# Kernel tuning notes

Measured on AMD Instinct MI355X. Metric: run time of the kernel, lower is better.

## Reference

```python
import jax, jax.numpy as jnp
import numpy as np

EPS = 1e-7  # tf.keras.backend.epsilon()


def squash(v, axis=-1):
    s = jnp.sum(jnp.square(v), axis=axis, keepdims=True)
    scale = s / (1.0 + s) / jnp.sqrt(s + EPS)
    return scale * v


def setup_inputs() -> dict:
    key = jax.random.key(0)
    k1, k2 = jax.random.split(key)
    B, I, D = 64, 2048, 16   # batch, input_num_capsule, input_dim_capsule
    J, K = 32, 16            # num_capsule, dim_capsule
    inputs = jax.random.normal(k1, (B, I, D), dtype=jnp.float32)
    # glorot_uniform-ish init for W: [in_caps, num_caps, in_dim, dim_caps]
    limit = np.sqrt(6.0 / (D + K)).astype(np.float32)
    W = jax.random.uniform(k2, (I, J, D, K), dtype=jnp.float32, minval=-limit, maxval=limit)
    return {"inputs": inputs, "W": W}


def reference(inputs, W, routings=3):
    # u_hat[b,i,j,:] = inputs[b,i,:] @ W[i,j,:,:]
    u_hat = jnp.einsum('bid,ijdk->bijk', inputs, W)  # [B, I, J, K]
    B, I, J, _ = u_hat.shape
    b = jnp.zeros((B, I, J, 1), dtype=u_hat.dtype)
    outputs = None
    for r in range(routings):
        c = jax.nn.softmax(b, axis=2)                              # [B, I, J, 1]
        outputs = squash(jnp.sum(c * u_hat, axis=1, keepdims=True))  # [B, 1, J, K]
        if r < routings - 1:
            b = b + jnp.sum(u_hat * outputs, axis=-1, keepdims=True)
    return jnp.squeeze(outputs, axis=1)  # [B, J, K]
```

## Files before the change

kernel.cpp:

```cpp
#include <hip/hip_runtime.h>
#include <hip/hip_bf16.h>


#define B_ 64
#define I_ 2048
#define D_ 16
#define J_ 32
#define K_ 16
#define JK 512

__device__ __forceinline__ float bf2f(unsigned int u) {
    union { unsigned int i; float f; } v;
    v.i = u << 16;
    return v.f;
}

__device__ __forceinline__ unsigned short f2bf(float f) {
    union { float f; unsigned int i; } v;
    v.f = f;
    const unsigned int x = v.i;
    return (unsigned short)((x + 0x7fffu + ((x >> 16) & 1u)) >> 16);
}

__device__ __forceinline__ void unpack8(const uint4 r, float* u) {
    u[0] = bf2f(r.x & 0xffffu); u[1] = bf2f(r.x >> 16);
    u[2] = bf2f(r.y & 0xffffu); u[3] = bf2f(r.y >> 16);
    u[4] = bf2f(r.z & 0xffffu); u[5] = bf2f(r.z >> 16);
    u[6] = bf2f(r.w & 0xffffu); u[7] = bf2f(r.w >> 16);
}

__global__ __launch_bounds__(64)
void caps_probe(const unsigned short* __restrict__ x, int* __restrict__ flag) {
    const int lane = threadIdx.x;
    int wild = 0;
#pragma unroll 8
    for (int t = 0; t < 128; ++t) {
        const unsigned int u = x[(size_t)lane * 128 + t];
        const unsigned int e = (u >> 7) & 0xffu;
        wild += (e >= 0xC0u) ? 1 : 0;
    }
    wild += __shfl_xor(wild, 1, 64);
    wild += __shfl_xor(wild, 2, 64);
    wild += __shfl_xor(wild, 4, 64);
    wild += __shfl_xor(wild, 8, 64);
    wild += __shfl_xor(wild, 16, 64);
    wild += __shfl_xor(wild, 32, 64);
    if (lane == 0) *flag = (wild > 32) ? 1 : 0;
}

__global__ __launch_bounds__(512)
void caps_produce(const void* __restrict__ xv, const void* __restrict__ Wv,
                  unsigned short* __restrict__ uhat, int b0, int BT,
                  const int* __restrict__ flag) {
    __shared__ float lx[4][64][D_];
    const int tid = threadIdx.x;
    const int g = tid >> 7;
    const int st = tid & 127;
    const int i = (blockIdx.x << 2) | g;
    const bool F32 = (*flag != 0);

    if (st < BT * 2) {
        const int bl = st >> 1, h = st & 1;
        float tmp[8];
        if (F32) {
            const float* xp =
                (const float*)xv + ((size_t)(b0 + bl) * I_ + i) * D_ + h * 8;
            const float4 r0 = reinterpret_cast<const float4*>(xp)[0];
            const float4 r1 = reinterpret_cast<const float4*>(xp)[1];
            tmp[0] = r0.x; tmp[1] = r0.y; tmp[2] = r0.z; tmp[3] = r0.w;
            tmp[4] = r1.x; tmp[5] = r1.y; tmp[6] = r1.z; tmp[7] = r1.w;
        } else {
            const uint4 r = *reinterpret_cast<const uint4*>(
                (const unsigned short*)xv +
                ((size_t)(b0 + bl) * I_ + i) * D_ + h * 8);
            unpack8(r, tmp);
        }
        float4* dst = reinterpret_cast<float4*>(&lx[g][bl][h * 8]);
        float4 d0, d1;
        d0.x = tmp[0]; d0.y = tmp[1]; d0.z = tmp[2]; d0.w = tmp[3];
        d1.x = tmp[4]; d1.y = tmp[5]; d1.z = tmp[6]; d1.w = tmp[7];
        dst[0] = d0; dst[1] = d1;
    }

    float w[16][4];
    {
        const int j = st >> 2, kh = st & 3;
        if (F32) {
            const float* wp = (const float*)Wv + (size_t)i * (J_ * D_ * K_) +
                              j * (D_ * K_) + kh * 4;
#pragma unroll
            for (int d = 0; d < 16; ++d) {
                const float4 r = *reinterpret_cast<const float4*>(wp + d * K_);
                w[d][0] = r.x; w[d][1] = r.y; w[d][2] = r.z; w[d][3] = r.w;
            }
        } else {
            const unsigned short* wp = (const unsigned short*)Wv +
                                       (size_t)i * (J_ * D_ * K_) +
                                       j * (D_ * K_) + kh * 4;
#pragma unroll
            for (int d = 0; d < 16; ++d) {
                const uint2 r = *reinterpret_cast<const uint2*>(wp + d * K_);
                w[d][0] = bf2f(r.x & 0xffffu); w[d][1] = bf2f(r.x >> 16);
                w[d][2] = bf2f(r.y & 0xffffu); w[d][3] = bf2f(r.y >> 16);
            }
        }
    }
    __syncthreads();

#pragma unroll 2
    for (int bl = 0; bl < BT; ++bl) {
        const float4* xr = reinterpret_cast<const float4*>(&lx[g][bl][0]);
        float a[4] = {0.f, 0.f, 0.f, 0.f};
#pragma unroll
        for (int dq = 0; dq < 4; ++dq) {
            const float4 xq = xr[dq];
            const float xs[4] = {xq.x, xq.y, xq.z, xq.w};
#pragma unroll
            for (int dd = 0; dd < 4; ++dd) {
#pragma unroll
                for (int c = 0; c < 4; ++c) a[c] += xs[dd] * w[dq * 4 + dd][c];
            }
        }
        uint2 pk;
        pk.x = ((unsigned int)f2bf(a[1]) << 16) | f2bf(a[0]);
        pk.y = ((unsigned int)f2bf(a[3]) << 16) | f2bf(a[2]);
        *reinterpret_cast<uint2*>(
            uhat + ((size_t)bl * I_ + i) * JK + st * 4) = pk;
    }
}

template <bool R0>
__global__ __launch_bounds__(256)
void caps_route(const unsigned short* __restrict__ uhat,
                const float* __restrict__ vsum,
                float* __restrict__ spart, int BT) {
    const int lane = threadIdx.x & 63;
    const int wave = blockIdx.x * 4 + (threadIdx.x >> 6);
    const int bl = wave >> 6;
    const int chunk = wave & 63;
    const int i0 = chunk * 32;

    float v[8];
    if (!R0) {
        const float4* vp =
            reinterpret_cast<const float4*>(vsum + bl * JK + lane * 8);
        const float4 v0 = vp[0], v1 = vp[1];
        v[0] = v0.x; v[1] = v0.y; v[2] = v0.z; v[3] = v0.w;
        v[4] = v1.x; v[5] = v1.y; v[6] = v1.z; v[7] = v1.w;
    }

    float acc[8] = {0.f, 0.f, 0.f, 0.f, 0.f, 0.f, 0.f, 0.f};
    const unsigned short* up = uhat + ((size_t)bl * I_ + i0) * JK + lane * 8;

#pragma unroll 2
    for (int ii = 0; ii < 32; ++ii) {
        const uint4 r = *reinterpret_cast<const uint4*>(up + (size_t)ii * JK);
        float u[8];
        unpack8(r, u);
        float c;
        if (R0) {
            c = 1.f;
        } else {
            float p = u[0] * v[0] + u[1] * v[1] + u[2] * v[2] + u[3] * v[3] +
                      u[4] * v[4] + u[5] * v[5] + u[6] * v[6] + u[7] * v[7];
            const float t = p + __shfl_xor(p, 1, 64);
            const float e = __expf(t);
            float S = e;
            S += __shfl_xor(S, 2, 64);
            S += __shfl_xor(S, 4, 64);
            S += __shfl_xor(S, 8, 64);
            S += __shfl_xor(S, 16, 64);
            S += __shfl_xor(S, 32, 64);
            c = e / S;
        }
#pragma unroll
        for (int q = 0; q < 8; ++q) acc[q] += c * u[q];
    }

    float* sp = spart + ((size_t)chunk * BT + bl) * JK + lane * 8;
    float4 o0, o1;
    o0.x = acc[0]; o0.y = acc[1]; o0.z = acc[2]; o0.w = acc[3];
    o1.x = acc[4]; o1.y = acc[5]; o1.z = acc[6]; o1.w = acc[7];
    reinterpret_cast<float4*>(sp)[0] = o0;
    reinterpret_cast<float4*>(sp)[1] = o1;
}

template <int MODE>
__global__ __launch_bounds__(512)
void caps_squash(const float* __restrict__ spart, float* __restrict__ vsum,
                 void* __restrict__ out, int b0, int BT,
                 const int* __restrict__ flag) {
    const int bl = blockIdx.x;
    const int jk = threadIdx.x;
    float s = 0.f;
#pragma unroll 8
    for (int p = 0; p < 64; ++p)
        s += spart[((size_t)p * BT + bl) * JK + jk];
    if (MODE == 0) s *= (1.f / 32.f);
    float q = s * s;
    q += __shfl_xor(q, 1, 64);
    q += __shfl_xor(q, 2, 64);
    q += __shfl_xor(q, 4, 64);
    q += __shfl_xor(q, 8, 64);
    const float scale = q / ((1.f + q) * sqrtf(q + 1e-7f));
    const float v = scale * s;
    if (MODE == 0)      vsum[bl * JK + jk] = v;
    else if (MODE == 1) vsum[bl * JK + jk] += v;
    else {
        const size_t o = (size_t)(b0 + bl) * JK + jk;
        if (*flag) ((float*)out)[o] = v;
        else       ((unsigned short*)out)[o] = f2bf(v);
    }
}

extern "C" void kernel_launch(void* const* d_in, const int* in_sizes, int n_in,
                              void* d_out, int out_size, void* d_ws,
                              size_t ws_size, hipStream_t stream) {
    const void* x = d_in[0];
    const void* W = d_in[1];
    char* ws = (char*)d_ws;

    int BT = 64;
    auto need = [](int bt) -> size_t {
        return (size_t)bt * I_ * JK * 2
             + (size_t)64 * bt * JK * 4
             + (size_t)bt * JK * 4
             + 256;
    };
    while (BT > 1 && need(BT) > ws_size) BT >>= 1;

    unsigned short* uhat = (unsigned short*)ws;
    float* spart = (float*)(ws + (size_t)BT * I_ * JK * 2);
    float* vsum = spart + (size_t)64 * BT * JK;
    int* flag = (int*)(vsum + (size_t)BT * JK);

    caps_probe<<<1, 64, 0, stream>>>((const unsigned short*)x, flag);

    const int NT = B_ / BT;
    for (int t = 0; t < NT; ++t) {
        const int b0 = t * BT;
        caps_produce<<<I_ / 4, 512, 0, stream>>>(x, W, uhat, b0, BT, flag);

        caps_route<true><<<BT * 16, 256, 0, stream>>>(uhat, vsum, spart, BT);
        caps_squash<0><<<BT, 512, 0, stream>>>(spart, vsum, d_out, b0, BT, flag);

        caps_route<false><<<BT * 16, 256, 0, stream>>>(uhat, vsum, spart, BT);
        caps_squash<1><<<BT, 512, 0, stream>>>(spart, vsum, d_out, b0, BT, flag);

        caps_route<false><<<BT * 16, 256, 0, stream>>>(uhat, vsum, spart, BT);
        caps_squash<2><<<BT, 512, 0, stream>>>(spart, vsum, d_out, b0, BT, flag);
    }
}
```

Before: 229.4 us.

## Drop LDS staging in produce and remap route lanes to whole capsules

The produce kernel no longer stages x through shared memory with a barrier. Each wave now loads the 16-element x row for its input capsule directly, using a readfirstlane-uniform index, and blocks shrink to 256 threads. The route kernel gives each lane a full 16-wide capsule j, with the two wave halves handling alternating i rows. This removes the pairwise shuffle for the dot product and folds the halves with one final shuffle. The trade-offs are more registers per lane, fewer concurrent i rows per block, and redundant x loads across lanes, which should be served as broadcasts.

New measurement: 245.7 us. 7.1% more time.

```diff
diff --git a/kernel.cpp b/kernel.cpp
--- a/kernel.cpp
+++ b/kernel.cpp
@@ -48,39 +48,16 @@
     if (lane == 0) *flag = (wild > 32) ? 1 : 0;
 }
 
-__global__ __launch_bounds__(512)
+__global__ __launch_bounds__(256)
 void caps_produce(const void* __restrict__ xv, const void* __restrict__ Wv,
                   unsigned short* __restrict__ uhat, int b0, int BT,
                   const int* __restrict__ flag) {
-    __shared__ float lx[4][64][D_];
     const int tid = threadIdx.x;
     const int g = tid >> 7;
     const int st = tid & 127;
-    const int i = (blockIdx.x << 2) | g;
+    int i = (blockIdx.x << 1) | g;
+    i = __builtin_amdgcn_readfirstlane(i);
     const bool F32 = (*flag != 0);
-
-    if (st < BT * 2) {
-        const int bl = st >> 1, h = st & 1;
-        float tmp[8];
-        if (F32) {
-            const float* xp =
-                (const float*)xv + ((size_t)(b0 + bl) * I_ + i) * D_ + h * 8;
-            const float4 r0 = reinterpret_cast<const float4*>(xp)[0];
-            const float4 r1 = reinterpret_cast<const float4*>(xp)[1];
-            tmp[0] = r0.x; tmp[1] = r0.y; tmp[2] = r0.z; tmp[3] = r0.w;
-            tmp[4] = r1.x; tmp[5] = r1.y; tmp[6] = r1.z; tmp[7] = r1.w;
-        } else {
-            const uint4 r = *reinterpret_cast<const uint4*>(
-                (const unsigned short*)xv +
-                ((size_t)(b0 + bl) * I_ + i) * D_ + h * 8);
-            unpack8(r, tmp);
-        }
-        float4* dst = reinterpret_cast<float4*>(&lx[g][bl][h * 8]);
-        float4 d0, d1;
-        d0.x = tmp[0]; d0.y = tmp[1]; d0.z = tmp[2]; d0.w = tmp[3];
-        d1.x = tmp[4]; d1.y = tmp[5]; d1.z = tmp[6]; d1.w = tmp[7];
-        dst[0] = d0; dst[1] = d1;
-    }
 
     float w[16][4];
     {
@@ -105,21 +82,34 @@
             }
         }
     }
-    __syncthreads();
-
-#pragma unroll 2
+
+#pragma unroll 4
     for (int bl = 0; bl < BT; ++bl) {
-        const float4* xr = reinterpret_cast<const float4*>(&lx[g][bl][0]);
+        float xs[16];
+        if (F32) {
+            const float* xp =
+                (const float*)xv + ((size_t)(b0 + bl) * I_ + i) * D_;
+            const float4 r0 = reinterpret_cast<const float4*>(xp)[0];
+            const float4 r1 = reinterpret_cast<const float4*>(xp)[1];
+            const float4 r2 = reinterpret_cast<const float4*>(xp)[2];
+            const float4 r3 = reinterpret_cast<const float4*>(xp)[3];
+            xs[0] = r0.x; xs[1] = r0.y; xs[2] = r0.z; xs[3] = r0.w;
+            xs[4] = r1.x; xs[5] = r1.y; xs[6] = r1.z; xs[7] = r1.w;
+            xs[8] = r2.x; xs[9] = r2.y; xs[10] = r2.z; xs[11] = r2.w;
+            xs[12] = r3.x; xs[13] = r3.y; xs[14] = r3.z; xs[15] = r3.w;
+        } else {
+            const unsigned short* xp =
+                (const unsigned short*)xv + ((size_t)(b0 + bl) * I_ + i) * D_;
+            const uint4 r0 = reinterpret_cast<const uint4*>(xp)[0];
+            const uint4 r1 = reinterpret_cast<const uint4*>(xp)[1];
+            unpack8(r0, xs);
+            unpack8(r1, xs + 8);
+        }
         float a[4] = {0.f, 0.f, 0.f, 0.f};
 #pragma unroll
-        for (int dq = 0; dq < 4; ++dq) {
-            const float4 xq = xr[dq];
-            const float xs[4] = {xq.x, xq.y, xq.z, xq.w};
-#pragma unroll
-            for (int dd = 0; dd < 4; ++dd) {
-#pragma unroll
-                for (int c = 0; c < 4; ++c) a[c] += xs[dd] * w[dq * 4 + dd][c];
-            }
+        for (int d = 0; d < 16; ++d) {
+#pragma unroll
+            for (int c = 0; c < 4; ++c) a[c] += xs[d] * w[d][c];
         }
         uint2 pk;
         pk.x = ((unsigned int)f2bf(a[1]) << 16) | f2bf(a[0]);
@@ -139,50 +129,68 @@
     const int bl = wave >> 6;
     const int chunk = wave & 63;
     const int i0 = chunk * 32;
-
-    float v[8];
+    const int h = lane >> 5;
+    const int j = lane & 31;
+
+    float v[16];
     if (!R0) {
         const float4* vp =
-            reinterpret_cast<const float4*>(vsum + bl * JK + lane * 8);
-        const float4 v0 = vp[0], v1 = vp[1];
-        v[0] = v0.x; v[1] = v0.y; v[2] = v0.z; v[3] = v0.w;
-        v[4] = v1.x; v[5] = v1.y; v[6] = v1.z; v[7] = v1.w;
-    }
-
-    float acc[8] = {0.f, 0.f, 0.f, 0.f, 0.f, 0.f, 0.f, 0.f};
-    const unsigned short* up = uhat + ((size_t)bl * I_ + i0) * JK + lane * 8;
+            reinterpret_cast<const float4*>(vsum + bl * JK + j * 16);
+        const float4 a0 = vp[0], a1 = vp[1], a2 = vp[2], a3 = vp[3];
+        v[0] = a0.x; v[1] = a0.y; v[2] = a0.z; v[3] = a0.w;
+        v[4] = a1.x; v[5] = a1.y; v[6] = a1.z; v[7] = a1.w;
+        v[8] = a2.x; v[9] = a2.y; v[10] = a2.z; v[11] = a2.w;
+        v[12] = a3.x; v[13] = a3.y; v[14] = a3.z; v[15] = a3.w;
+    }
+
+    float acc[16];
+#pragma unroll
+    for (int k = 0; k < 16; ++k) acc[k] = 0.f;
+
+    const unsigned short* up =
+        uhat + ((size_t)bl * I_ + i0 + h) * JK + j * 16;
 
 #pragma unroll 2
-    for (int ii = 0; ii < 32; ++ii) {
-        const uint4 r = *reinterpret_cast<const uint4*>(up + (size_t)ii * JK);
-        float u[8];
-        unpack8(r, u);
+    for (int t = 0; t < 16; ++t) {
+        const uint4* rp =
+            reinterpret_cast<const uint4*>(up + (size_t)t * 2 * JK);
+        const uint4 r0 = rp[0], r1 = rp[1];
+        float u[16];
+        unpack8(r0, u);
+        unpack8(r1, u + 8);
         float c;
         if (R0) {
             c = 1.f;
         } else {
-            float p = u[0] * v[0] + u[1] * v[1] + u[2] * v[2] + u[3] * v[3] +
-                      u[4] * v[4] + u[5] * v[5] + u[6] * v[6] + u[7] * v[7];
-            const float t = p + __shfl_xor(p, 1, 64);
-            const float e = __expf(t);
+            float p = 0.f;
+#pragma unroll
+            for (int k = 0; k < 16; ++k) p += u[k] * v[k];
+            const float e = __expf(p);
             float S = e;
+            S += __shfl_xor(S, 1, 64);
             S += __shfl_xor(S, 2, 64);
             S += __shfl_xor(S, 4, 64);
             S += __shfl_xor(S, 8, 64);
             S += __shfl_xor(S, 16, 64);
-            S += __shfl_xor(S, 32, 64);
-            c = e / S;
-        }
-#pragma unroll
-        for (int q = 0; q < 8; ++q) acc[q] += c * u[q];
-    }
-
-    float* sp = spart + ((size_t)chunk * BT + bl) * JK + lane * 8;
-    float4 o0, o1;
-    o0.x = acc[0]; o0.y = acc[1]; o0.z = acc[2]; o0.w = acc[3];
-    o1.x = acc[4]; o1.y = acc[5]; o1.z = acc[6]; o1.w = acc[7];
-    reinterpret_cast<float4*>(sp)[0] = o0;
-    reinterpret_cast<float4*>(sp)[1] = o1;
+            c = e / (S + 1e-30f);
+        }
+#pragma unroll
+        for (int k = 0; k < 16; ++k) acc[k] += c * u[k];
+    }
+
+#pragma unroll
+    for (int k = 0; k < 16; ++k) acc[k] += __shfl_xor(acc[k], 32, 64);
+
+    if (h == 0) {
+        float* sp = spart + ((size_t)chunk * BT + bl) * JK + j * 16;
+        float4 o;
+#pragma unroll
+        for (int q = 0; q < 4; ++q) {
+            o.x = acc[q * 4 + 0]; o.y = acc[q * 4 + 1];
+            o.z = acc[q * 4 + 2]; o.w = acc[q * 4 + 3];
+            reinterpret_cast<float4*>(sp)[q] = o;
+        }
+    }
 }
 
 template <int MODE>
@@ -239,7 +247,7 @@
     const int NT = B_ / BT;
     for (int t = 0; t < NT; ++t) {
         const int b0 = t * BT;
-        caps_produce<<<I_ / 4, 512, 0, stream>>>(x, W, uhat, b0, BT, flag);
+        caps_produce<<<I_ / 2, 256, 0, stream>>>(x, W, uhat, b0, BT, flag);
 
         caps_route<true><<<BT * 16, 256, 0, stream>>>(uhat, vsum, spart, BT);
         caps_squash<0><<<BT, 512, 0, stream>>>(spart, vsum, d_out, b0, BT, flag);
```
